# Performance work log

Hardware: AMD Instinct MI355X
Metric: run time of the kernel (lower is better)

The kernel has to match this reference:

```python
import jax, jax.numpy as jnp
import numpy as np

EMB = 1024
HEADS = 16
HEADSIZE = EMB // HEADS
EPS = 1e-5  # torch LayerNorm default


def _layernorm(x, g, b):
    # normalize over last dim (headsize)
    m = jnp.mean(x, axis=-1, keepdims=True)
    v = jnp.mean((x - m) ** 2, axis=-1, keepdims=True)
    return (x - m) * jax.lax.rsqrt(v + EPS) * g + b


def setup_inputs() -> dict:
    key = jax.random.key(0)
    ks = jax.random.split(key, 6)
    B, T = 4, 2048
    s = 1.0 / np.sqrt(EMB)  # ~ torch Linear init scale
    return {
        "x": jax.random.normal(ks[0], (B, T, EMB), dtype=jnp.float32),
        "Wk": jax.random.normal(ks[1], (EMB, EMB), dtype=jnp.float32) * s,
        "Wq": jax.random.normal(ks[2], (EMB, EMB), dtype=jnp.float32) * s,
        "Wv": jax.random.normal(ks[3], (EMB, EMB), dtype=jnp.float32) * s,
        "Wo": jax.random.normal(ks[4], (EMB, EMB), dtype=jnp.float32) * s,
        "bo": jnp.zeros((EMB,), dtype=jnp.float32),
        "kln_g": jnp.ones((HEADSIZE,), dtype=jnp.float32),
        "kln_b": jnp.zeros((HEADSIZE,), dtype=jnp.float32),
        "qln_g": jnp.ones((HEADSIZE,), dtype=jnp.float32),
        "qln_b": jnp.zeros((HEADSIZE,), dtype=jnp.float32),
    }


def reference(x, Wk, Wq, Wv, Wo, bo, kln_g, kln_b, qln_g, qln_b):
    B, T, E = x.shape
    # projections (torch Linear: y = x @ W.T), split into heads
    k = jnp.einsum("bte,fe->btf", x, Wk).reshape(B, T, HEADS, HEADSIZE)
    q = jnp.einsum("bte,fe->btf", x, Wq).reshape(B, T, HEADS, HEADSIZE)
    v = jnp.einsum("bte,fe->btf", x, Wv).reshape(B, T, HEADS, HEADSIZE)
    # optional per-head layernorm on keys/queries (kqnorm=True)
    k = _layernorm(k, kln_g, kln_b)
    q = _layernorm(q, qln_g, qln_b)
    # note: original scales by emb**-1/4 on each of q and k (total 1/sqrt(emb))
    scale = E ** (-0.25)
    q = q * scale
    k = k * scale
    # full [B, H, T, T] score matrix (faithful to bmm implementation)
    dot = jnp.einsum("bihd,bjhd->bhij", q, k)
    # causal mask: j > i set to -inf (mask_diagonal=False -> offset=1)
    causal = jnp.triu(jnp.ones((T, T), dtype=bool), k=1)
    dot = jnp.where(causal, -jnp.inf, dot)
    att = jax.nn.softmax(dot, axis=-1)
    out = jnp.einsum("bhij,bjhd->bihd", att, v).reshape(B, T, E)
    return jnp.einsum("bte,fe->btf", out, Wo) + bo
```

## Files before the change

kernel.cpp:

```cpp
#include <hip/hip_runtime.h>
#include <hip/hip_bf16.h>
#include <cstdint>

#define EMB 1024
#define HEADS 16
#define HD 64
#define BATCH 4
#define SEQ 2048
#define BT (BATCH*SEQ)
#define LNEPS 1e-5f
#define QK_SCALE 0.17677669529663687f
#define LOG2E 1.4426950408889634f

typedef __bf16 bf16;
typedef __bf16 bf16x8 __attribute__((ext_vector_type(8)));
typedef __bf16 bf16x4 __attribute__((ext_vector_type(4)));
typedef float  f32x4  __attribute__((ext_vector_type(4)));
typedef short  s16x4  __attribute__((ext_vector_type(4)));

typedef const __attribute__((address_space(1))) void* gas_ptr;
typedef __attribute__((address_space(3))) void*       las_ptr;

__device__ __forceinline__ void gld_lds16(const void* g, void* l) {
  __builtin_amdgcn_global_load_lds((gas_ptr)g, (las_ptr)l, 16, 0, 0);
}

__device__ __forceinline__ f32x4 mfma_pv(bf16x4 a, bf16x4 b, f32x4 c) {
  return __builtin_amdgcn_mfma_f32_16x16x16bf16_1k(
      __builtin_bit_cast(s16x4, a), __builtin_bit_cast(s16x4, b), c, 0, 0, 0);
}

__global__ void cvt_all(const float* __restrict__ x,
                        const float* __restrict__ w0, const float* __restrict__ w1,
                        const float* __restrict__ w2, const float* __restrict__ w3,
                        bf16* __restrict__ xb, bf16* __restrict__ wb) {
  const int bid = blockIdx.x;
  if (bid < 8192) {
    int i = bid * 256 + threadIdx.x;
    float4 f = reinterpret_cast<const float4*>(x)[i];
    bf16x4 o = { (bf16)f.x, (bf16)f.y, (bf16)f.z, (bf16)f.w };
    reinterpret_cast<bf16x4*>(xb)[i] = o;
  } else {
    int i = (bid - 8192) * 256 + threadIdx.x;
    int sel = i >> 18;
    int j = i & 262143;
    const float* s = (sel == 0) ? w0 : (sel == 1) ? w1 : (sel == 2) ? w2 : w3;
    float4 f = reinterpret_cast<const float4*>(s)[j];
    bf16x4 o = { (bf16)f.x, (bf16)f.y, (bf16)f.z, (bf16)f.w };
    reinterpret_cast<bf16x4*>(wb)[i] = o;
  }
}

template<int OUTF32>
__global__ __launch_bounds__(256, 2) void gemm_bt(
    const bf16* __restrict__ A, const bf16* __restrict__ Bm,
    bf16* __restrict__ Cb, float* __restrict__ Cf, const float* __restrict__ bias,
    int M, int N, int K)
{
  __shared__ __align__(16) bf16 As[128 * 32];
  __shared__ __align__(16) bf16 Bs[128 * 32];

  const int t    = threadIdx.x;
  const int lane = t & 63;
  const int wave = t >> 6;
  const int q    = lane >> 4;
  const int ln   = lane & 15;

  const int lid = (int)blockIdx.y * (int)gridDim.x + (int)blockIdx.x;
  const int xcd = lid & 7;
  const int nn  = lid >> 3;
  const int bxr = nn >> 3;
  const int byr = (xcd << 3) | (nn & 7);
  const int m0  = byr * 128;
  const int n0  = bxr * 128;

  const int wm   = (wave >> 1) * 64;
  const int wn   = (wave & 1) * 64;

  const int r0 = t >> 2;
  const int c0 = (t & 3) << 3;

  f32x4 zero4 = {0.f, 0.f, 0.f, 0.f};
  f32x4 acc[4][4];
#pragma unroll
  for (int i = 0; i < 4; i++)
#pragma unroll
    for (int j = 0; j < 4; j++) acc[i][j] = zero4;

  for (int k0 = 0; k0 < K; k0 += 32) {
    __syncthreads();
    const bf16* ga = A  + (size_t)(m0 + r0) * K + k0 + c0;
    const bf16* gb = Bm + (size_t)(n0 + r0) * K + k0 + c0;
    gld_lds16(ga,                  &As[t * 8]);
    gld_lds16(ga + (size_t)64 * K, &As[t * 8 + 2048]);
    gld_lds16(gb,                  &Bs[t * 8]);
    gld_lds16(gb + (size_t)64 * K, &Bs[t * 8 + 2048]);
    __syncthreads();

    bf16x8 af[4], bfr[4];
#pragma unroll
    for (int mi = 0; mi < 4; mi++)
      af[mi] = *reinterpret_cast<const bf16x8*>(&As[(wm + mi * 16 + ln) * 32 + q * 8]);
#pragma unroll
    for (int ni = 0; ni < 4; ni++)
      bfr[ni] = *reinterpret_cast<const bf16x8*>(&Bs[(wn + ni * 16 + ln) * 32 + q * 8]);
#pragma unroll
    for (int mi = 0; mi < 4; mi++)
#pragma unroll
      for (int ni = 0; ni < 4; ni++)
        acc[mi][ni] = __builtin_amdgcn_mfma_f32_16x16x32_bf16(af[mi], bfr[ni], acc[mi][ni], 0, 0, 0);
  }

#pragma unroll
  for (int mi = 0; mi < 4; mi++) {
#pragma unroll
    for (int ni = 0; ni < 4; ni++) {
#pragma unroll
      for (int r = 0; r < 4; r++) {
        int row = m0 + wm + mi * 16 + q * 4 + r;
        int col = n0 + wn + ni * 16 + ln;
        float v = acc[mi][ni][r];
        if (OUTF32) Cf[(size_t)row * N + col] = v + bias[col];
        else        Cb[(size_t)row * N + col] = (bf16)v;
      }
    }
  }
}

__global__ void ln_vt(const bf16* __restrict__ kqv,
                      bf16* __restrict__ kn, bf16* __restrict__ qn,
                      bf16* __restrict__ vt,
                      const float* __restrict__ kg, const float* __restrict__ kb,
                      const float* __restrict__ qg, const float* __restrict__ qb,
                      float kscale, float qscale)
{
  __shared__ __align__(16) bf16 tile[64][72];
  const int bid = blockIdx.x;
  const int t = threadIdx.x;
  if (bid < 4096) {
    const int lr = t & 7;
    const int row = bid * 32 + (t >> 3);
    const int tok = row >> 4, h = row & 15;
    const size_t base = (size_t)tok * (3 * EMB) + h * HD + lr * 8;

    bf16x8 vk = *reinterpret_cast<const bf16x8*>(kqv + base);
    bf16x8 vq = *reinterpret_cast<const bf16x8*>(kqv + base + EMB);

    float fk[8], fq[8];
    float sk = 0.f, sq = 0.f, s2k = 0.f, s2q = 0.f;
#pragma unroll
    for (int e = 0; e < 8; e++) {
      fk[e] = (float)vk[e]; fq[e] = (float)vq[e];
      sk += fk[e]; sq += fq[e];
      s2k += fk[e] * fk[e]; s2q += fq[e] * fq[e];
    }
#pragma unroll
    for (int m = 1; m < 8; m <<= 1) {
      sk  += __shfl_xor(sk,  m, 64); sq  += __shfl_xor(sq,  m, 64);
      s2k += __shfl_xor(s2k, m, 64); s2q += __shfl_xor(s2q, m, 64);
    }
    float mk = sk * (1.f / 64.f), mq = sq * (1.f / 64.f);
    float rk = rsqrtf(s2k * (1.f / 64.f) - mk * mk + LNEPS) * kscale;
    float rq = rsqrtf(s2q * (1.f / 64.f) - mq * mq + LNEPS) * qscale;

    bf16x8 ok, oq;
#pragma unroll
    for (int e = 0; e < 8; e++) {
      float gk = kg[lr * 8 + e], bk2 = kb[lr * 8 + e];
      float gq = qg[lr * 8 + e], bq2 = qb[lr * 8 + e];
      ok[e] = (bf16)(((fk[e] - mk) * rk) * gk + bk2 * kscale);
      oq[e] = (bf16)(((fq[e] - mq) * rq) * gq + bq2 * qscale);
    }
    const int b = tok >> 11, tt = tok & 2047;
    const size_t o = ((size_t)(b * HEADS + h) * SEQ + tt) * HD + lr * 8;
    *reinterpret_cast<bf16x8*>(kn + o) = ok;
    *reinterpret_cast<bf16x8*>(qn + o) = oq;
  } else {
    const int idx = bid - 4096;
    const int jt = idx & 31, bh = idx >> 5;
    const int b = bh >> 4, h = bh & 15;
    const bf16* in = kqv + 2 * EMB;
#pragma unroll
    for (int p = 0; p < 2; p++) {
      int rowj = p * 32 + (t >> 3);
      int cold = (t & 7) << 3;
      bf16x8 v = *reinterpret_cast<const bf16x8*>(
          &in[(size_t)(b * SEQ + jt * 64 + rowj) * (3 * EMB) + h * HD + cold]);
      *reinterpret_cast<bf16x8*>(&tile[rowj][cold]) = v;
    }
    __syncthreads();
#pragma unroll
    for (int p = 0; p < 2; p++) {
      int rowd = p * 32 + (t >> 3);
      int colj = (t & 7) << 3;
      bf16x8 v;
#pragma unroll
      for (int jj = 0; jj < 8; jj++) v[jj] = tile[colj + jj][rowd];
      *reinterpret_cast<bf16x8*>(&vt[((size_t)bh * HD + rowd) * SEQ + jt * 64 + colj]) = v;
    }
  }
}

__global__ __launch_bounds__(256, 4) void attn(
    const bf16* __restrict__ Qn, const bf16* __restrict__ Kn, const bf16* __restrict__ Vt,
    bf16* __restrict__ O)
{
  __shared__ __align__(16) bf16 Ks[2][64 * 64];
  __shared__ __align__(16) bf16 Vs[2][64 * 64];

  const int id = blockIdx.x;
  const int bh = ((id >> 7) << 3) | (id & 7);
  const int bxi = (id >> 3) & 15;
  const int t = threadIdx.x, wave = t >> 6, lane = t & 63;
  const int q = lane >> 4, ln = lane & 15;
  const int b = bh >> 4, h = bh & 15;

  const int u0 = t * 8, u1 = t * 8 + 2048;
  const int kr0 = u0 >> 6, kc0 = ((u0 >> 3) & 7) ^ (kr0 & 7);
  const int kr1 = u1 >> 6, kc1 = ((u1 >> 3) & 7) ^ (kr1 & 7);
  const int vd0 = u0 >> 6, vc0 = ((u0 >> 3) & 7) ^ (vd0 & 7);
  const int vd1 = u1 >> 6, vc1 = ((u1 >> 3) & 7) ^ (vd1 & 7);
  const bf16* Kb = Kn + (size_t)bh * SEQ * HD;
  const bf16* Vb = Vt + (size_t)bh * HD * SEQ;

  f32x4 zero4 = {0.f, 0.f, 0.f, 0.f};

  for (int pass = 0; pass < 2; ++pass) {
    const int itile = pass ? (31 - bxi) : bxi;
    const int qbase = itile * 64 + wave * 16;

    const bf16* qp = Qn + ((size_t)bh * SEQ + qbase + ln) * HD + q * 8;
    bf16x8 qf0 = *reinterpret_cast<const bf16x8*>(qp);
    bf16x8 qf1 = *reinterpret_cast<const bf16x8*>(qp + 32);

    float lrow = 0.f;
    f32x4 oacc[4];
#pragma unroll
    for (int md = 0; md < 4; md++) oacc[md] = zero4;

    const int nj = itile + 1;

    __syncthreads();
    {
      gld_lds16(Kb + (size_t)kr0 * HD + kc0 * 8, &Ks[0][u0]);
      gld_lds16(Kb + (size_t)kr1 * HD + kc1 * 8, &Ks[0][u1]);
      gld_lds16(Vb + (size_t)vd0 * SEQ + vc0 * 8, &Vs[0][u0]);
      gld_lds16(Vb + (size_t)vd1 * SEQ + vc1 * 8, &Vs[0][u1]);
    }

    for (int jt = 0; jt < nj; ++jt) {
      const int buf = jt & 1;
      const int j0 = jt * 64;
      __syncthreads();
      if (jt + 1 < nj) {
        const int jn = j0 + 64;
        gld_lds16(Kb + (size_t)(jn + kr0) * HD + kc0 * 8, &Ks[buf ^ 1][u0]);
        gld_lds16(Kb + (size_t)(jn + kr1) * HD + kc1 * 8, &Ks[buf ^ 1][u1]);
        gld_lds16(Vb + (size_t)vd0 * SEQ + jn + vc0 * 8, &Vs[buf ^ 1][u0]);
        gld_lds16(Vb + (size_t)vd1 * SEQ + jn + vc1 * 8, &Vs[buf ^ 1][u1]);
      }

#pragma unroll
      for (int jb = 0; jb < 4; ++jb) {
        const int jslab = j0 + jb * 16;
        if (jslab <= qbase + 15) {
          const int rowj = jb * 16 + ln;
          bf16x8 kf0 = *reinterpret_cast<const bf16x8*>(
              &Ks[buf][rowj * 64 + ((q)     ^ (rowj & 7)) * 8]);
          bf16x8 kf1 = *reinterpret_cast<const bf16x8*>(
              &Ks[buf][rowj * 64 + ((4 + q) ^ (rowj & 7)) * 8]);
          f32x4 z = zero4;
          z = __builtin_amdgcn_mfma_f32_16x16x32_bf16(kf0, qf0, z, 0, 0, 0);
          z = __builtin_amdgcn_mfma_f32_16x16x32_bf16(kf1, qf1, z, 0, 0, 0);
          if (jslab + 15 > qbase) {
#pragma unroll
            for (int r = 0; r < 4; r++) {
              int jj = jslab + q * 4 + r;
              int ii = qbase + ln;
              if (jj > ii) z[r] = -1.0e30f;
            }
          }
          float p0 = exp2f(z[0]), p1 = exp2f(z[1]), p2 = exp2f(z[2]), p3 = exp2f(z[3]);
          lrow += (p0 + p1) + (p2 + p3);
          bf16x4 pk = { (bf16)p0, (bf16)p1, (bf16)p2, (bf16)p3 };

#pragma unroll
          for (int md = 0; md < 4; md++) {
            const int rowd = md * 16 + ln;
            const bf16* vp = &Vs[buf][rowd * 64 +
                (((jb * 2 + (q >> 1)) ^ (rowd & 7)) * 8) + (q & 1) * 4];
            bf16x4 vf = *reinterpret_cast<const bf16x4*>(vp);
            oacc[md] = mfma_pv(vf, pk, oacc[md]);
          }
        }
      }
    }

    float s = lrow;
    s += __shfl_xor(s, 16, 64);
    s += __shfl_xor(s, 32, 64);
    const float inv = 1.f / s;
    const int row = qbase + ln;
#pragma unroll
    for (int md = 0; md < 4; md++) {
      bf16x4 o4 = { (bf16)(oacc[md][0] * inv), (bf16)(oacc[md][1] * inv),
                    (bf16)(oacc[md][2] * inv), (bf16)(oacc[md][3] * inv) };
      int col = h * HD + md * 16 + q * 4;
      *reinterpret_cast<bf16x4*>(&O[(size_t)(b * SEQ + row) * EMB + col]) = o4;
    }
  }
}

extern "C" void kernel_launch(void* const* d_in, const int* in_sizes, int n_in,
                              void* d_out, int out_size, void* d_ws, size_t ws_size,
                              hipStream_t stream)
{
  const float* x   = (const float*)d_in[0];
  const float* Wk  = (const float*)d_in[1];
  const float* Wq  = (const float*)d_in[2];
  const float* Wv  = (const float*)d_in[3];
  const float* Wo  = (const float*)d_in[4];
  const float* bo  = (const float*)d_in[5];
  const float* klg = (const float*)d_in[6];
  const float* klb = (const float*)d_in[7];
  const float* qlg = (const float*)d_in[8];
  const float* qlb = (const float*)d_in[9];
  float* out = (float*)d_out;

  char* ws = (char*)d_ws;
  const size_t OFF_XB  = 0;
  const size_t OFF_WB  = OFF_XB  + (size_t)BT * EMB * 2;
  const size_t OFF_KQV = OFF_WB  + (size_t)4 * EMB * EMB * 2;
  const size_t OFF_KN  = OFF_KQV + (size_t)BT * 3 * EMB * 2;
  const size_t OFF_QN  = OFF_KN  + (size_t)BT * EMB * 2;
  const size_t OFF_VT  = OFF_QN  + (size_t)BT * EMB * 2;
  const size_t OFF_END = OFF_VT  + (size_t)BT * EMB * 2;
  if (ws_size < OFF_END) return;

  bf16* xb   = (bf16*)(ws + OFF_XB);
  bf16* wb   = (bf16*)(ws + OFF_WB);
  bf16* kqv  = (bf16*)(ws + OFF_KQV);
  bf16* kn   = (bf16*)(ws + OFF_KN);
  bf16* qn   = (bf16*)(ws + OFF_QN);
  bf16* vt   = (bf16*)(ws + OFF_VT);
  bf16* ob   = (bf16*)(ws + OFF_KQV);

  cvt_all<<<12288, 256, 0, stream>>>(x, Wk, Wq, Wv, Wo, xb, wb);

  gemm_bt<0><<<dim3(3 * EMB / 128, BT / 128), 256, 0, stream>>>(
      xb, wb, kqv, (float*)nullptr, (const float*)nullptr, BT, 3 * EMB, EMB);

  ln_vt<<<4096 + 2048, 256, 0, stream>>>(kqv, kn, qn, vt, klg, klb, qlg, qlb,
                                         QK_SCALE * LOG2E, QK_SCALE);

  attn<<<dim3(16 * BATCH * HEADS), 256, 0, stream>>>(qn, kn, vt, ob);

  gemm_bt<1><<<dim3(EMB / 128, BT / 128), 256, 0, stream>>>(
      ob, wb + (size_t)3 * EMB * EMB, (bf16*)nullptr, out, bo, BT, EMB, EMB);
}
```

Measured before the change: 279.8 us.

## Fuse per-head LayerNorm and V transpose into the KQV projection GEMM epilogue

Adds a dedicated KQV GEMM whose epilogue applies per-head LayerNorm and scaling to K and Q using cross-lane shuffles, and writes V directly in transposed layout. This removes the separate ln_vt kernel and the round trip of the bf16 KQV intermediate through global memory. In exchange the epilogue stores are narrower and more scattered (scalar bf16 stores for K/Q, strided bf16x4 for V), and the epilogue adds shuffle work inside the GEMM.

```diff
diff --git a/kernel.cpp b/kernel.cpp
--- a/kernel.cpp
+++ b/kernel.cpp
@@ -51,6 +51,123 @@
   }
 }
 
+__global__ __launch_bounds__(256, 2) void gemm_kqv(
+    const bf16* __restrict__ A, const bf16* __restrict__ Bm,
+    bf16* __restrict__ kn, bf16* __restrict__ qn, bf16* __restrict__ vt,
+    const float* __restrict__ kg, const float* __restrict__ kb,
+    const float* __restrict__ qg, const float* __restrict__ qb)
+{
+  __shared__ __align__(16) bf16 As[128 * 32];
+  __shared__ __align__(16) bf16 Bs[128 * 32];
+
+  const int K = EMB;
+  const int t    = threadIdx.x;
+  const int lane = t & 63;
+  const int wave = t >> 6;
+  const int q    = lane >> 4;
+  const int ln   = lane & 15;
+
+  const int lid = (int)blockIdx.y * (int)gridDim.x + (int)blockIdx.x;
+  const int xcd = lid & 7;
+  const int nn  = lid >> 3;
+  const int bxr = nn >> 3;
+  const int byr = (xcd << 3) | (nn & 7);
+  const int m0  = byr * 128;
+  const int n0  = bxr * 128;
+
+  const int wm = (wave >> 1) * 64;
+  const int wn = (wave & 1) * 64;
+
+  const int r0 = t >> 2;
+  const int c0 = (t & 3) << 3;
+
+  f32x4 zero4 = {0.f, 0.f, 0.f, 0.f};
+  f32x4 acc[4][4];
+#pragma unroll
+  for (int i = 0; i < 4; i++)
+#pragma unroll
+    for (int j = 0; j < 4; j++) acc[i][j] = zero4;
+
+  for (int k0 = 0; k0 < K; k0 += 32) {
+    __syncthreads();
+    const bf16* ga = A  + (size_t)(m0 + r0) * K + k0 + c0;
+    const bf16* gb = Bm + (size_t)(n0 + r0) * K + k0 + c0;
+    gld_lds16(ga,                  &As[t * 8]);
+    gld_lds16(ga + (size_t)64 * K, &As[t * 8 + 2048]);
+    gld_lds16(gb,                  &Bs[t * 8]);
+    gld_lds16(gb + (size_t)64 * K, &Bs[t * 8 + 2048]);
+    __syncthreads();
+
+    bf16x8 af[4], bfr[4];
+#pragma unroll
+    for (int mi = 0; mi < 4; mi++)
+      af[mi] = *reinterpret_cast<const bf16x8*>(&As[(wm + mi * 16 + ln) * 32 + q * 8]);
+#pragma unroll
+    for (int ni = 0; ni < 4; ni++)
+      bfr[ni] = *reinterpret_cast<const bf16x8*>(&Bs[(wn + ni * 16 + ln) * 32 + q * 8]);
+#pragma unroll
+    for (int mi = 0; mi < 4; mi++)
+#pragma unroll
+      for (int ni = 0; ni < 4; ni++)
+        acc[mi][ni] = __builtin_amdgcn_mfma_f32_16x16x32_bf16(af[mi], bfr[ni], acc[mi][ni], 0, 0, 0);
+  }
+
+  const int sec = n0 >> 10;
+  const int cb  = (n0 & 1023) + wn;
+  const int h   = cb >> 6;
+  const int R0  = m0 + wm;
+
+  if (sec == 2) {
+#pragma unroll
+    for (int mi = 0; mi < 4; mi++) {
+      const int R = R0 + mi * 16 + q * 4;
+      const int b = R >> 11, tt = R & 2047;
+#pragma unroll
+      for (int ni = 0; ni < 4; ni++) {
+        const int d = ni * 16 + ln;
+        bf16x4 o4 = { (bf16)acc[mi][ni][0], (bf16)acc[mi][ni][1],
+                      (bf16)acc[mi][ni][2], (bf16)acc[mi][ni][3] };
+        *reinterpret_cast<bf16x4*>(
+            &vt[((size_t)(b * HEADS + h) * HD + d) * SEQ + tt]) = o4;
+      }
+    }
+  } else {
+    const float scale = sec ? QK_SCALE : (QK_SCALE * LOG2E);
+    const float* gp = sec ? qg : kg;
+    const float* bp = sec ? qb : kb;
+    bf16* outp = sec ? qn : kn;
+    float gv[4], bv[4];
+#pragma unroll
+    for (int ni = 0; ni < 4; ni++) {
+      gv[ni] = gp[ni * 16 + ln];
+      bv[ni] = bp[ni * 16 + ln] * scale;
+    }
+#pragma unroll
+    for (int mi = 0; mi < 4; mi++) {
+#pragma unroll
+      for (int r = 0; r < 4; r++) {
+        const float x0 = acc[mi][0][r], x1 = acc[mi][1][r];
+        const float x2 = acc[mi][2][r], x3 = acc[mi][3][r];
+        float s  = (x0 + x1) + (x2 + x3);
+        float s2 = (x0 * x0 + x1 * x1) + (x2 * x2 + x3 * x3);
+#pragma unroll
+        for (int mm = 1; mm < 16; mm <<= 1) {
+          s  += __shfl_xor(s,  mm, 64);
+          s2 += __shfl_xor(s2, mm, 64);
+        }
+        const float mean = s * (1.f / 64.f);
+        const float rs = rsqrtf(s2 * (1.f / 64.f) - mean * mean + LNEPS) * scale;
+        const int R = R0 + mi * 16 + q * 4 + r;
+        const int b = R >> 11, tt = R & 2047;
+        const size_t o = ((size_t)(b * HEADS + h) * SEQ + tt) * HD + ln;
+#pragma unroll
+        for (int ni = 0; ni < 4; ni++)
+          outp[o + ni * 16] = (bf16)((acc[mi][ni][r] - mean) * rs * gv[ni] + bv[ni]);
+      }
+    }
+  }
+}
+
 template<int OUTF32>
 __global__ __launch_bounds__(256, 2) void gemm_bt(
     const bf16* __restrict__ A, const bf16* __restrict__ Bm,
@@ -123,80 +240,6 @@
         if (OUTF32) Cf[(size_t)row * N + col] = v + bias[col];
         else        Cb[(size_t)row * N + col] = (bf16)v;
       }
-    }
-  }
-}
-
-__global__ void ln_vt(const bf16* __restrict__ kqv,
-                      bf16* __restrict__ kn, bf16* __restrict__ qn,
-                      bf16* __restrict__ vt,
-                      const float* __restrict__ kg, const float* __restrict__ kb,
-                      const float* __restrict__ qg, const float* __restrict__ qb,
-                      float kscale, float qscale)
-{
-  __shared__ __align__(16) bf16 tile[64][72];
-  const int bid = blockIdx.x;
-  const int t = threadIdx.x;
-  if (bid < 4096) {
-    const int lr = t & 7;
-    const int row = bid * 32 + (t >> 3);
-    const int tok = row >> 4, h = row & 15;
-    const size_t base = (size_t)tok * (3 * EMB) + h * HD + lr * 8;
-
-    bf16x8 vk = *reinterpret_cast<const bf16x8*>(kqv + base);
-    bf16x8 vq = *reinterpret_cast<const bf16x8*>(kqv + base + EMB);
-
-    float fk[8], fq[8];
-    float sk = 0.f, sq = 0.f, s2k = 0.f, s2q = 0.f;
-#pragma unroll
-    for (int e = 0; e < 8; e++) {
-      fk[e] = (float)vk[e]; fq[e] = (float)vq[e];
-      sk += fk[e]; sq += fq[e];
-      s2k += fk[e] * fk[e]; s2q += fq[e] * fq[e];
-    }
-#pragma unroll
-    for (int m = 1; m < 8; m <<= 1) {
-      sk  += __shfl_xor(sk,  m, 64); sq  += __shfl_xor(sq,  m, 64);
-      s2k += __shfl_xor(s2k, m, 64); s2q += __shfl_xor(s2q, m, 64);
-    }
-    float mk = sk * (1.f / 64.f), mq = sq * (1.f / 64.f);
-    float rk = rsqrtf(s2k * (1.f / 64.f) - mk * mk + LNEPS) * kscale;
-    float rq = rsqrtf(s2q * (1.f / 64.f) - mq * mq + LNEPS) * qscale;
-
-    bf16x8 ok, oq;
-#pragma unroll
-    for (int e = 0; e < 8; e++) {
-      float gk = kg[lr * 8 + e], bk2 = kb[lr * 8 + e];
-      float gq = qg[lr * 8 + e], bq2 = qb[lr * 8 + e];
-      ok[e] = (bf16)(((fk[e] - mk) * rk) * gk + bk2 * kscale);
-      oq[e] = (bf16)(((fq[e] - mq) * rq) * gq + bq2 * qscale);
-    }
-    const int b = tok >> 11, tt = tok & 2047;
-    const size_t o = ((size_t)(b * HEADS + h) * SEQ + tt) * HD + lr * 8;
-    *reinterpret_cast<bf16x8*>(kn + o) = ok;
-    *reinterpret_cast<bf16x8*>(qn + o) = oq;
-  } else {
-    const int idx = bid - 4096;
-    const int jt = idx & 31, bh = idx >> 5;
-    const int b = bh >> 4, h = bh & 15;
-    const bf16* in = kqv + 2 * EMB;
-#pragma unroll
-    for (int p = 0; p < 2; p++) {
-      int rowj = p * 32 + (t >> 3);
-      int cold = (t & 7) << 3;
-      bf16x8 v = *reinterpret_cast<const bf16x8*>(
-          &in[(size_t)(b * SEQ + jt * 64 + rowj) * (3 * EMB) + h * HD + cold]);
-      *reinterpret_cast<bf16x8*>(&tile[rowj][cold]) = v;
-    }
-    __syncthreads();
-#pragma unroll
-    for (int p = 0; p < 2; p++) {
-      int rowd = p * 32 + (t >> 3);
-      int colj = (t & 7) << 3;
-      bf16x8 v;
-#pragma unroll
-      for (int jj = 0; jj < 8; jj++) v[jj] = tile[colj + jj][rowd];
-      *reinterpret_cast<bf16x8*>(&vt[((size_t)bh * HD + rowd) * SEQ + jt * 64 + colj]) = v;
     }
   }
 }
@@ -339,7 +382,6 @@
 
   bf16* xb   = (bf16*)(ws + OFF_XB);
   bf16* wb   = (bf16*)(ws + OFF_WB);
-  bf16* kqv  = (bf16*)(ws + OFF_KQV);
   bf16* kn   = (bf16*)(ws + OFF_KN);
   bf16* qn   = (bf16*)(ws + OFF_QN);
   bf16* vt   = (bf16*)(ws + OFF_VT);
@@ -347,11 +389,8 @@
 
   cvt_all<<<12288, 256, 0, stream>>>(x, Wk, Wq, Wv, Wo, xb, wb);
 
-  gemm_bt<0><<<dim3(3 * EMB / 128, BT / 128), 256, 0, stream>>>(
-      xb, wb, kqv, (float*)nullptr, (const float*)nullptr, BT, 3 * EMB, EMB);
-
-  ln_vt<<<4096 + 2048, 256, 0, stream>>>(kqv, kn, qn, vt, klg, klb, qlg, qlb,
-                                         QK_SCALE * LOG2E, QK_SCALE);
+  gemm_kqv<<<dim3(3 * EMB / 128, BT / 128), 256, 0, stream>>>(
+      xb, wb, kn, qn, vt, klg, klb, qlg, qlb);
 
   attn<<<dim3(16 * BATCH * HEADS), 256, 0, stream>>>(qn, kn, vt, ob);
 
```

Measured after the change: 267.2 us. -4.5%, faster.
